# Kernel tuning notes

Measured on AMD Instinct MI355X. Metric: run time of the kernel, lower is better.

The kernel has to match this reference:

```python
import jax, jax.numpy as jnp
import numpy as np

EMBED_DIM = 1024
LN_EPS = 1e-5


def _layernorm(x, w, b):
    m = jnp.mean(x, axis=-1, keepdims=True)
    v = jnp.mean(jnp.square(x - m), axis=-1, keepdims=True)
    return (x - m) * jax.lax.rsqrt(v + LN_EPS) * w + b


def _attention(q, k, v, scale):
    # q: [b, sq, d], k/v: [b, sk, d]
    scores = jnp.einsum('bqd,bkd->bqk', q, k) * scale
    probs = jax.nn.softmax(scores, axis=-1)
    return jnp.einsum('bqk,bkd->bqd', probs, v)


def setup_inputs() -> dict:
    key = jax.random.key(0)
    ks = jax.random.split(key, 16)
    B, SQ, SK, D, H = 8, 577, 13271, EMBED_DIM, 4  # H=int(4.0) per source
    return {
        'input_features': jax.random.normal(ks[0], (B, SK, D), jnp.float32),
        'query_feature': jax.random.normal(ks[1], (B, SQ, D), jnp.float32),
        'norm1_w': jax.random.uniform(ks[2], (D,), jnp.float32, 0.5, 1.5),
        'norm1_b': jax.random.normal(ks[3], (D,), jnp.float32) * 0.1,
        'norm2_w': jax.random.uniform(ks[4], (D,), jnp.float32, 0.5, 1.5),
        'norm2_b': jax.random.normal(ks[5], (D,), jnp.float32) * 0.1,
        'norm3_w': jax.random.uniform(ks[6], (D,), jnp.float32, 0.5, 1.5),
        'norm3_b': jax.random.normal(ks[7], (D,), jnp.float32) * 0.1,
        'gamma1': jax.random.uniform(ks[8], (D,), jnp.float32, 0.5, 1.5),
        'gamma2': jax.random.uniform(ks[9], (D,), jnp.float32, 0.5, 1.5),
        'fc1_w': jax.random.normal(ks[10], (H, D), jnp.float32) * (1.0 / np.sqrt(D)),
        'fc1_b': jax.random.normal(ks[11], (H,), jnp.float32) * 0.01,
        'fc2_w': jax.random.normal(ks[12], (D, H), jnp.float32) * (1.0 / np.sqrt(H)),
        'fc2_b': jax.random.normal(ks[13], (D,), jnp.float32) * 0.01,
    }


def reference(input_features, query_feature, norm1_w, norm1_b, norm2_w, norm2_b,
              norm3_w, norm3_b, gamma1, gamma2, fc1_w, fc1_b, fc2_w, fc2_b):
    scale = EMBED_DIM ** (-0.5)
    norm_X = _layernorm(input_features, norm1_w, norm1_b)
    norm_F_L = _layernorm(query_feature, norm2_w, norm2_b)
    # cross attention: query = last-layer feats, key/value = concat of earlier layers
    attended = _attention(norm_F_L, norm_X, norm_X, scale)
    # MLP with exact-erf GELU (torch nn.GELU default), dropout=0 -> identity
    h = jax.nn.gelu(attended @ fc1_w.T + fc1_b, approximate=False)
    cross_attended = h @ fc2_w.T + fc2_b
    norm_cross = _layernorm(cross_attended, norm3_w, norm3_b)
    self_attended = _attention(norm_cross, norm_cross, norm_cross, scale)
    skip_connect = cross_attended + gamma1 * self_attended
    return norm_F_L + gamma2 * skip_connect
```

## Files before the change

### kernel.cpp

```cpp
#include <hip/hip_runtime.h>
#include <hip/hip_bf16.h>
#include <math.h>

typedef unsigned short u16;
typedef __attribute__((ext_vector_type(4))) unsigned short u16x4;
typedef __attribute__((ext_vector_type(8))) __bf16 bf16x8;
typedef __attribute__((ext_vector_type(4))) float fx4;

#define DEV __device__ __forceinline__

DEV u16 f2bf(float f) {
    unsigned u = __float_as_uint(f);
    u += 0x7fffu + ((u >> 16) & 1u);
    return (u16)(u >> 16);
}

DEV void async_load16(const void* g, void* l) {
    __builtin_amdgcn_global_load_lds(
        (const __attribute__((address_space(1))) void*)g,
        (__attribute__((address_space(3))) void*)l, 16, 0, 0);
}

DEV void block_reduce2(float& a, float& b) {
    #pragma unroll
    for (int o = 32; o; o >>= 1) { a += __shfl_xor(a, o); b += __shfl_xor(b, o); }
    __shared__ float sa[4], sb[4];
    const int lane = threadIdx.x & 63, wv = threadIdx.x >> 6;
    if (lane == 0) { sa[wv] = a; sb[wv] = b; }
    __syncthreads();
    a = sa[0] + sa[1] + sa[2] + sa[3];
    b = sb[0] + sb[1] + sb[2] + sb[3];
    __syncthreads();
}

DEV void xcd_swizzle3(int& bx, int& by, int& bz) {
    const int nx = gridDim.x, ny = gridDim.y;
    const int total = nx * ny * gridDim.z;
    const int lin = blockIdx.x + nx * (blockIdx.y + ny * blockIdx.z);
    if (total & 7) { bx = blockIdx.x; by = blockIdx.y; bz = blockIdx.z; return; }
    const int cpx = total >> 3;
    const int swz = (lin & 7) * cpx + (lin >> 3);
    bx = swz % nx;
    const int r = swz / nx;
    by = r % ny;
    bz = r / ny;
}

__global__ __launch_bounds__(256) void ln_wave_k(
    const float* __restrict__ in, int rows_real, int rows_pad,
    const float* __restrict__ w, const float* __restrict__ bias,
    u16* __restrict__ out_bf, float* __restrict__ out_f32, float out_scale)
{
    const int wv = threadIdx.x >> 6, lane = threadIdx.x & 63;
    const int r = blockIdx.x * 4 + wv, b = blockIdx.y;
    const size_t orow = ((size_t)b * rows_pad + r) * 1024 + lane * 4;
    if (r >= rows_real) {
        u16x4 z = {0, 0, 0, 0};
        fx4 zf = {0.f, 0.f, 0.f, 0.f};
        #pragma unroll
        for (int c = 0; c < 4; ++c) {
            *(u16x4*)&out_bf[orow + c * 256] = z;
            if (out_f32) *(fx4*)&out_f32[orow + c * 256] = zf;
        }
        return;
    }
    const size_t irow = ((size_t)b * rows_real + r) * 1024 + lane * 4;
    fx4 x[4];
    float s1 = 0.f, s2 = 0.f;
    #pragma unroll
    for (int c = 0; c < 4; ++c) {
        x[c] = *(const fx4*)&in[irow + c * 256];
        s1 += x[c].x + x[c].y + x[c].z + x[c].w;
        s2 += x[c].x * x[c].x + x[c].y * x[c].y + x[c].z * x[c].z + x[c].w * x[c].w;
    }
    #pragma unroll
    for (int o = 32; o; o >>= 1) { s1 += __shfl_xor(s1, o); s2 += __shfl_xor(s2, o); }
    const float m = s1 * (1.0f / 1024.0f);
    const float var = s2 * (1.0f / 1024.0f) - m * m;
    const float rs = rsqrtf(var + 1e-5f);
    #pragma unroll
    for (int c = 0; c < 4; ++c) {
        fx4 wv4 = *(const fx4*)&w[c * 256 + lane * 4];
        fx4 bv4 = *(const fx4*)&bias[c * 256 + lane * 4];
        fx4 y;
        y.x = (x[c].x - m) * rs * wv4.x + bv4.x;
        y.y = (x[c].y - m) * rs * wv4.y + bv4.y;
        y.z = (x[c].z - m) * rs * wv4.z + bv4.z;
        y.w = (x[c].w - m) * rs * wv4.w + bv4.w;
        u16x4 o = { f2bf(y.x * out_scale), f2bf(y.y * out_scale),
                    f2bf(y.z * out_scale), f2bf(y.w * out_scale) };
        *(u16x4*)&out_bf[orow + c * 256] = o;
        if (out_f32) *(fx4*)&out_f32[orow + c * 256] = y;
    }
}

template<bool ATOMIC>
DEV void gemm_body(
    const u16* __restrict__ Ab, const u16* __restrict__ Bb, float* __restrict__ Cb,
    int k_begin, int iters, int lda, int ldb, int ldc)
{
    __shared__ u16 lA[2][128 * 32];
    __shared__ u16 lB[2][128 * 32];
    const int lane = threadIdx.x & 63, wv = threadIdx.x >> 6;
    const int wm = (wv >> 1) * 64, wn = (wv & 1) * 64;
    const int frow = lane & 15, quad = lane >> 4;

    fx4 acc[4][4];
    #pragma unroll
    for (int i = 0; i < 4; ++i)
        #pragma unroll
        for (int j = 0; j < 4; ++j) { acc[i][j].x = 0; acc[i][j].y = 0; acc[i][j].z = 0; acc[i][j].w = 0; }

    const int c0 = wv * 64 + lane;
    const int r0a = c0 >> 2, s0 = (c0 & 3) * 8;
    const int c1 = 256 + c0;
    const int r1a = c1 >> 2, s1 = (c1 & 3) * 8;

    auto stage = [&](int buf, int it) {
        const int k0 = k_begin + it * 32;
        async_load16(Ab + (size_t)r0a * lda + k0 + s0, &lA[buf][(wv * 64) * 8]);
        async_load16(Ab + (size_t)r1a * lda + k0 + s1, &lA[buf][(256 + wv * 64) * 8]);
        async_load16(Bb + (size_t)r0a * ldb + k0 + s0, &lB[buf][(wv * 64) * 8]);
        async_load16(Bb + (size_t)r1a * ldb + k0 + s1, &lB[buf][(256 + wv * 64) * 8]);
    };

    stage(0, 0);
    __syncthreads();
    int cur = 0;
    for (int it = 0; it < iters; ++it) {
        if (it + 1 < iters) stage(cur ^ 1, it + 1);
        bf16x8 af[4], bfr[4];
        #pragma unroll
        for (int i = 0; i < 4; ++i) {
            af[i]  = *(const bf16x8*)&lA[cur][(wm + i * 16 + frow) * 32 + quad * 8];
            bfr[i] = *(const bf16x8*)&lB[cur][(wn + i * 16 + frow) * 32 + quad * 8];
        }
        #pragma unroll
        for (int mi = 0; mi < 4; ++mi)
            #pragma unroll
            for (int ni = 0; ni < 4; ++ni)
                acc[mi][ni] = __builtin_amdgcn_mfma_f32_16x16x32_bf16(af[mi], bfr[ni], acc[mi][ni], 0, 0, 0);
        __syncthreads();
        cur ^= 1;
    }

    #pragma unroll
    for (int mi = 0; mi < 4; ++mi) {
        #pragma unroll
        for (int r = 0; r < 4; ++r) {
            const int row = wm + mi * 16 + quad * 4 + r;
            #pragma unroll
            for (int ni = 0; ni < 4; ++ni) {
                const int col = wn + ni * 16 + frow;
                if (ATOMIC) atomicAdd(&Cb[(size_t)row * ldc + col], acc[mi][ni][r]);
                else        Cb[(size_t)row * ldc + col] = acc[mi][ni][r];
            }
        }
    }
}

template<int NS>
__global__ __launch_bounds__(256) void gemm_bt_sk(
    const u16* __restrict__ A, const u16* __restrict__ B, float* __restrict__ C,
    int iters_per, int lda, int ldb, int ldc, long As, long Bs, long Cs)
{
    int bx, by, bzz;
    xcd_swizzle3(bx, by, bzz);
    const int bz = bzz / NS, sp = bzz % NS;
    const u16* Ab = A + (size_t)bz * As + (size_t)by * 128 * lda;
    const u16* Bb = B + (size_t)bz * Bs + (size_t)bx * 128 * ldb;
    float* Cb = C + (size_t)bz * Cs + (size_t)by * 128 * ldc + (size_t)bx * 128;
    gemm_body<true>(Ab, Bb, Cb, sp * iters_per * 32, iters_per, lda, ldb, ldc);
}

template<bool ATOMIC>
DEV void gemm256_body(
    const u16* __restrict__ A, const u16* __restrict__ B, float* __restrict__ C,
    int k_begin, int NT, int lda, int ldb, int ldc, int bx, int by, int Mreal)
{
    __shared__ u16 lds[2][4][8192];
    const int tid = threadIdx.x;
    const int lane = tid & 63, wid = tid >> 6;
    const int wr = wid >> 2, wc = wid & 3;
    const int frow = lane & 15, quad = lane >> 4;
    const int sw = (frow & 7) << 4;
    const int csrc = ((lane & 7) ^ ((lane >> 3) & 7)) * 8;
    const int by256 = by * 256, bx256 = bx * 256;
    const int mclamp = Mreal - 1;

    fx4 acc[8][4];
    #pragma unroll
    for (int i = 0; i < 8; ++i)
        #pragma unroll
        for (int j = 0; j < 4; ++j) { acc[i][j].x = 0; acc[i][j].y = 0; acc[i][j].z = 0; acc[i][j].w = 0; }

    auto stageA = [&](int buf, int half, int ktile) {
        const int kcol = k_begin + ktile * 64;
        #pragma unroll
        for (int j = 0; j < 2; ++j) {
            int grow = by256 + half * 128 + (wid * 2 + j) * 8 + (lane >> 3);
            if (grow > mclamp) grow = mclamp;
            async_load16(A + (size_t)grow * lda + kcol + csrc,
                         &lds[buf][half][(wid * 2 + j) * 512]);
        }
    };
    auto stageB = [&](int buf, int half, int ktile) {
        const int kcol = k_begin + ktile * 64;
        #pragma unroll
        for (int j = 0; j < 2; ++j) {
            const int grow = bx256 + half * 128 + (wid * 2 + j) * 8 + (lane >> 3);
            async_load16(B + (size_t)grow * ldb + kcol + csrc,
                         &lds[buf][2 + half][(wid * 2 + j) * 512]);
        }
    };

#define DO_PHASE(MQ, NQ, STAGE_STMT, WAITN)                                              \
    {                                                                                    \
        STAGE_STMT;                                                                      \
        __builtin_amdgcn_sched_barrier(0);                                               \
        asm volatile("s_waitcnt vmcnt(" #WAITN ")" ::: "memory");                        \
        __builtin_amdgcn_s_barrier();                                                    \
        __builtin_amdgcn_sched_barrier(0);                                               \
        const char* pa = (const char*)&lds[cur][MQ][0];                                  \
        const char* pb = (const char*)&lds[cur][2 + NQ][0];                              \
        bf16x8 av[4][2], bv[2][2];                                                       \
        _Pragma("unroll")                                                                \
        for (int f = 0; f < 4; ++f) {                                                    \
            const int row = wr * 64 + f * 16 + frow;                                     \
            _Pragma("unroll")                                                            \
            for (int ks = 0; ks < 2; ++ks)                                               \
                av[f][ks] = *(const bf16x8*)(pa + row * 128 + ((((ks * 4 + quad) << 4)) ^ sw)); \
        }                                                                                \
        _Pragma("unroll")                                                                \
        for (int gg = 0; gg < 2; ++gg) {                                                 \
            const int col = wc * 32 + gg * 16 + frow;                                    \
            _Pragma("unroll")                                                            \
            for (int ks = 0; ks < 2; ++ks)                                               \
                bv[gg][ks] = *(const bf16x8*)(pb + col * 128 + ((((ks * 4 + quad) << 4)) ^ sw)); \
        }                                                                                \
        __builtin_amdgcn_s_setprio(1);                                                   \
        _Pragma("unroll")                                                                \
        for (int f = 0; f < 4; ++f)                                                      \
            _Pragma("unroll")                                                            \
            for (int gg = 0; gg < 2; ++gg)                                               \
                _Pragma("unroll")                                                        \
                for (int ks = 0; ks < 2; ++ks)                                           \
                    acc[MQ * 4 + f][NQ * 2 + gg] = __builtin_amdgcn_mfma_f32_16x16x32_bf16( \
                        av[f][ks], bv[gg][ks], acc[MQ * 4 + f][NQ * 2 + gg], 0, 0, 0);   \
        __builtin_amdgcn_s_setprio(0);                                                   \
    }

    stageA(0, 0, 0);
    stageB(0, 0, 0);
    stageB(0, 1, 0);
    stageA(0, 1, 0);
    stageA(1, 0, 1);

    int cur = 0;
    for (int t = 0; t <= NT - 2; ++t) {
        const int nxt = cur ^ 1;
        DO_PHASE(0, 0, stageB(nxt, 0, t + 1), 8)
        DO_PHASE(0, 1, stageB(nxt, 1, t + 1), 8)
        DO_PHASE(1, 0, stageA(nxt, 1, t + 1), 8)
        DO_PHASE(1, 1, if (t + 2 < NT) stageA(cur, 0, t + 2), 8)
        cur = nxt;
    }
    DO_PHASE(0, 0, (void)0, 4)
    DO_PHASE(0, 1, (void)0, 2)
    DO_PHASE(1, 0, (void)0, 0)
    DO_PHASE(1, 1, (void)0, 0)
#undef DO_PHASE

    #pragma unroll
    for (int mf = 0; mf < 8; ++mf) {
        const int rowb = (mf >> 2) * 128 + wr * 64 + (mf & 3) * 16 + quad * 4;
        #pragma unroll
        for (int r = 0; r < 4; ++r) {
            const int grow = by256 + rowb + r;
            if (grow < Mreal) {
                #pragma unroll
                for (int nf = 0; nf < 4; ++nf) {
                    const int gcol = bx256 + (nf >> 1) * 128 + wc * 32 + (nf & 1) * 16 + frow;
                    if (ATOMIC) atomicAdd(&C[(size_t)grow * ldc + gcol], acc[mf][nf][r]);
                    else C[(size_t)grow * ldc + gcol] = acc[mf][nf][r];
                }
            }
        }
    }
}

__global__ __launch_bounds__(512, 2) void gemm256_qk(
    const u16* __restrict__ A, const u16* __restrict__ B, float* __restrict__ C,
    int NT, int lda, int ldb, int ldc, long As, long Bs, long Cs, int Mreal)
{
    const int lin = blockIdx.x + gridDim.x * (blockIdx.y + gridDim.y * blockIdx.z);
    const int per_bx = gridDim.y * gridDim.z;
    const int bx = lin / per_bx, rem = lin % per_bx;
    const int by = rem % gridDim.y, bz = rem / gridDim.y;
    gemm256_body<false>(A + (size_t)bz * As, B + (size_t)bz * Bs, C + (size_t)bz * Cs,
                        0, NT, lda, ldb, ldc, bx, by, Mreal);
}

template<int NS>
__global__ __launch_bounds__(512, 2) void gemm256_sk(
    const u16* __restrict__ A, const u16* __restrict__ B, float* __restrict__ C,
    int NT_per, int lda, int ldb, int ldc, long As, long Bs, long Cs, int Mreal)
{
    int bx, by, bzz;
    xcd_swizzle3(bx, by, bzz);
    const int bz = bzz / NS, sp = bzz % NS;
    gemm256_body<true>(A + (size_t)bz * As, B + (size_t)bz * Bs, C + (size_t)bz * Cs,
                       sp * NT_per * 64, NT_per, lda, ldb, ldc, bx, by, Mreal);
}

template<int EPT4>
__global__ __launch_bounds__(256) void softmax_k(
    const float* __restrict__ S, u16* __restrict__ P,
    int n_real, int n_pad, float scale, long Ss, long Ps)
{
    const int tid = threadIdx.x;
    const float* Sr = S + (size_t)blockIdx.y * Ss + (size_t)blockIdx.x * n_pad;
    u16* Pr = P + (size_t)blockIdx.y * Ps + (size_t)blockIdx.x * n_pad;
    fx4 v[EPT4];
    float mx = -INFINITY;
    #pragma unroll
    for (int i = 0; i < EPT4; ++i) {
        const int base = (i * 256 + tid) * 4;
        fx4 s;
        if (base < n_pad) s = *(const fx4*)&Sr[base];
        else { s.x = -INFINITY; s.y = -INFINITY; s.z = -INFINITY; s.w = -INFINITY; }
        s.x = (base + 0 < n_real) ? s.x * scale : -INFINITY;
        s.y = (base + 1 < n_real) ? s.y * scale : -INFINITY;
        s.z = (base + 2 < n_real) ? s.z * scale : -INFINITY;
        s.w = (base + 3 < n_real) ? s.w * scale : -INFINITY;
        v[i] = s;
        mx = fmaxf(mx, fmaxf(fmaxf(s.x, s.y), fmaxf(s.z, s.w)));
    }
    #pragma unroll
    for (int o = 32; o; o >>= 1) mx = fmaxf(mx, __shfl_xor(mx, o));
    __shared__ float sm[4];
    const int lane = tid & 63, wvi = tid >> 6;
    if (lane == 0) sm[wvi] = mx;
    __syncthreads();
    mx = fmaxf(fmaxf(sm[0], sm[1]), fmaxf(sm[2], sm[3]));
    __syncthreads();
    float sum = 0.f;
    #pragma unroll
    for (int i = 0; i < EPT4; ++i) {
        fx4 e;
        e.x = __expf(v[i].x - mx); e.y = __expf(v[i].y - mx);
        e.z = __expf(v[i].z - mx); e.w = __expf(v[i].w - mx);
        v[i] = e;
        sum += e.x + e.y + e.z + e.w;
    }
    #pragma unroll
    for (int o = 32; o; o >>= 1) sum += __shfl_xor(sum, o);
    if (lane == 0) sm[wvi] = sum;
    __syncthreads();
    sum = sm[0] + sm[1] + sm[2] + sm[3];
    const float inv = 1.0f / sum;
    #pragma unroll
    for (int i = 0; i < EPT4; ++i) {
        const int base = (i * 256 + tid) * 4;
        if (base < n_pad) {
            u16x4 o = { f2bf(v[i].x * inv), f2bf(v[i].y * inv),
                        f2bf(v[i].z * inv), f2bf(v[i].w * inv) };
            *(u16x4*)&Pr[base] = o;
        }
    }
}

__global__ __launch_bounds__(256) void transpose_k(
    const u16* __restrict__ in, u16* __restrict__ out,
    int in_rows, int in_cols, long is, long os)
{
    __shared__ u16 t[64][68];
    const int b = blockIdx.z;
    const u16* I = in + (size_t)b * is;
    u16* O = out + (size_t)b * os;
    const int c0 = blockIdx.x * 64, r0 = blockIdx.y * 64;
    const int cx = threadIdx.x & 15, ry = threadIdx.x >> 4;
    u16x4 a[4];
    #pragma unroll
    for (int k = 0; k < 4; ++k)
        a[k] = *(const u16x4*)&I[(size_t)(r0 + 4 * ry + k) * in_cols + c0 + 4 * cx];
    #pragma unroll
    for (int e = 0; e < 4; ++e) {
        u16x4 o = { a[0][e], a[1][e], a[2][e], a[3][e] };
        *(u16x4*)&t[4 * cx + e][4 * ry] = o;
    }
    __syncthreads();
    #pragma unroll
    for (int k = 0; k < 4; ++k) {
        const int oc = 4 * ry + k;
        *(u16x4*)&O[(size_t)(c0 + oc) * in_rows + r0 + 4 * cx] =
            *(const u16x4*)&t[oc][4 * cx];
    }
}

__global__ __launch_bounds__(256) void mlp_ln_k(
    const float* __restrict__ att, const float* __restrict__ w1, const float* __restrict__ b1,
    const float* __restrict__ w2, const float* __restrict__ b2,
    const float* __restrict__ w3, const float* __restrict__ b3,
    float* __restrict__ ca, u16* __restrict__ nc, int rows_real)
{
    const int q = blockIdx.x, b = blockIdx.y, tid = threadIdx.x;
    const size_t row = ((size_t)b * gridDim.x + q) * 1024 + tid * 4;
    if (q >= rows_real) {
        fx4 zf = {0.f, 0.f, 0.f, 0.f}; u16x4 z = {0, 0, 0, 0};
        *(fx4*)&ca[row] = zf;
        *(u16x4*)&nc[row] = z;
        return;
    }
    fx4 x = *(const fx4*)&att[row];
    float p[4];
    #pragma unroll
    for (int j = 0; j < 4; ++j) {
        fx4 wj = *(const fx4*)&w1[j * 1024 + tid * 4];
        p[j] = x.x * wj.x + x.y * wj.y + x.z * wj.z + x.w * wj.w;
        #pragma unroll
        for (int o = 32; o; o >>= 1) p[j] += __shfl_xor(p[j], o);
    }
    __shared__ float sh[4][4];
    const int lane = tid & 63, wvi = tid >> 6;
    if (lane == 0) { sh[wvi][0] = p[0]; sh[wvi][1] = p[1]; sh[wvi][2] = p[2]; sh[wvi][3] = p[3]; }
    __syncthreads();
    float h[4];
    #pragma unroll
    for (int j = 0; j < 4; ++j) {
        float s = sh[0][j] + sh[1][j] + sh[2][j] + sh[3][j] + b1[j];
        h[j] = 0.5f * s * (1.0f + erff(s * 0.70710678118f));
    }
    float v[4]; float s1 = 0.f, s2 = 0.f;
    #pragma unroll
    for (int e = 0; e < 4; ++e) {
        const int d = tid * 4 + e;
        fx4 wd = *(const fx4*)&w2[d * 4];
        float t = h[0] * wd.x + h[1] * wd.y + h[2] * wd.z + h[3] * wd.w + b2[d];
        v[e] = t; s1 += t; s2 += t * t;
    }
    block_reduce2(s1, s2);
    const float m = s1 * (1.0f / 1024.0f);
    const float var = s2 * (1.0f / 1024.0f) - m * m;
    const float rs = rsqrtf(var + 1e-5f);
    fx4 cav = {v[0], v[1], v[2], v[3]};
    *(fx4*)&ca[row] = cav;
    fx4 w3v = *(const fx4*)&w3[tid * 4], b3v = *(const fx4*)&b3[tid * 4];
    u16x4 o = { f2bf((v[0] - m) * rs * w3v.x + b3v.x), f2bf((v[1] - m) * rs * w3v.y + b3v.y),
                f2bf((v[2] - m) * rs * w3v.z + b3v.z), f2bf((v[3] - m) * rs * w3v.w + b3v.w) };
    *(u16x4*)&nc[row] = o;
}

__global__ __launch_bounds__(256) void final_k(
    const float* __restrict__ nF, const float* __restrict__ ca,
    const float* __restrict__ att2, const float* __restrict__ g1,
    const float* __restrict__ g2, float* __restrict__ out, int sq, int sqp)
{
    const int q = blockIdx.x, b = blockIdx.y, tid = threadIdx.x;
    const size_t wrow = ((size_t)b * sqp + q) * 1024 + tid * 4;
    const size_t orow = ((size_t)b * sq + q) * 1024 + tid * 4;
    fx4 nf = *(const fx4*)&nF[wrow];
    fx4 c  = *(const fx4*)&ca[wrow];
    fx4 a2 = *(const fx4*)&att2[wrow];
    fx4 G1 = *(const fx4*)&g1[tid * 4];
    fx4 G2 = *(const fx4*)&g2[tid * 4];
    fx4 r;
    r.x = nf.x + G2.x * (c.x + G1.x * a2.x);
    r.y = nf.y + G2.y * (c.y + G1.y * a2.y);
    r.z = nf.z + G2.z * (c.z + G1.z * a2.z);
    r.w = nf.w + G2.w * (c.w + G1.w * a2.w);
    *(fx4*)&out[orow] = r;
}

extern "C" void kernel_launch(void* const* d_in, const int* in_sizes, int n_in,
                              void* d_out, int out_size, void* d_ws, size_t ws_size,
                              hipStream_t stream) {
    const float* x_in = (const float*)d_in[0];
    const float* q_in = (const float*)d_in[1];
    const float* n1w = (const float*)d_in[2];
    const float* n1b = (const float*)d_in[3];
    const float* n2w = (const float*)d_in[4];
    const float* n2b = (const float*)d_in[5];
    const float* n3w = (const float*)d_in[6];
    const float* n3b = (const float*)d_in[7];
    const float* g1  = (const float*)d_in[8];
    const float* g2  = (const float*)d_in[9];
    const float* w1  = (const float*)d_in[10];
    const float* b1  = (const float*)d_in[11];
    const float* w2  = (const float*)d_in[12];
    const float* b2  = (const float*)d_in[13];
    float* out = (float*)d_out;

    const int B = 8, SQ = 577, SK = 13271, D = 1024;
    const int SQP = 640, SKP = 13312;
    const float scale = 0.03125f;

    char* ws = (char*)d_ws;
    size_t off = 0;
    auto alloc = [&](size_t n) { size_t o = off; off = (off + n + 255) & ~(size_t)255; return o; };
    u16*   Xn   = (u16*)  (ws + alloc((size_t)B * SKP * D * 2));
    u16*   Xt   = (u16*)  (ws + alloc((size_t)B * D * SKP * 2));
    u16*   Qb   = (u16*)  (ws + alloc((size_t)B * SQP * D * 2));
    float* nF   = (float*)(ws + alloc((size_t)B * SQP * D * 4));
    u16*   P    = (u16*)  (ws + alloc((size_t)B * SQP * SKP * 2));
    float* att  = (float*)(ws + alloc((size_t)B * SQP * D * 4));
    float* CA   = (float*)(ws + alloc((size_t)B * SQP * D * 4));
    u16*   NC   = (u16*)  (ws + alloc((size_t)B * SQP * D * 2));
    u16*   NCt  = (u16*)  (ws + alloc((size_t)B * D * SQP * 2));
    float* S2   = (float*)(ws + alloc((size_t)B * SQP * SQP * 4));
    u16*   P2   = (u16*)  (ws + alloc((size_t)B * SQP * SQP * 2));
    float* att2 = (float*)(ws + alloc((size_t)B * SQP * D * 4));
    const size_t perS1 = (size_t)SQP * SKP * 4;
    size_t room = (ws_size > off) ? (ws_size - off) / perS1 : 1;
    int g = (int)(room < 1 ? 1 : (room > 4 ? 4 : room));
    float* S1 = (float*)(ws + off);
    (void)in_sizes; (void)n_in; (void)out_size;

    ln_wave_k<<<dim3(SKP / 4, B), 256, 0, stream>>>(x_in, SK, SKP, n1w, n1b, Xn, nullptr, 1.0f);
    ln_wave_k<<<dim3(SQP / 4, B), 256, 0, stream>>>(q_in, SQ, SQP, n2w, n2b, Qb, nF, scale);

    transpose_k<<<dim3(D / 64, SKP / 64, B), 256, 0, stream>>>(
        Xn, Xt, SKP, D, (long)SKP * D, (long)SKP * D);

    for (int b = 0; b < B; b += g) {
        const int nb = (B - b) < g ? (B - b) : g;
        gemm256_qk<<<dim3(SKP / 256, 3, nb), 512, 0, stream>>>(
            Qb + (size_t)b * SQP * D, Xn + (size_t)b * SKP * D, S1,
            D / 64, D, D, SKP, (long)SQP * D, (long)SKP * D, (long)SQP * SKP, SQP);
        softmax_k<13><<<dim3(SQP, nb), 256, 0, stream>>>(
            S1, P + (size_t)b * SQP * SKP, SK, SKP, 1.0f,
            (long)SQP * SKP, (long)SQP * SKP);
    }

    hipMemsetAsync(att, 0, (size_t)B * SQP * D * 4, stream);
    gemm256_sk<8><<<dim3(D / 256, 3, B * 8), 512, 0, stream>>>(
        P, Xt, att, (SKP / 64) / 8, SKP, SKP, D,
        (long)SQP * SKP, (long)D * SKP, (long)SQP * D, SQP);

    mlp_ln_k<<<dim3(SQP, B), 256, 0, stream>>>(att, w1, b1, w2, b2, n3w, n3b, CA, NC, SQ);

    transpose_k<<<dim3(D / 64, SQP / 64, B), 256, 0, stream>>>(
        NC, NCt, SQP, D, (long)SQP * D, (long)SQP * D);
    hipMemsetAsync(S2, 0, (size_t)B * SQP * SQP * 4, stream);
    gemm_bt_sk<2><<<dim3(SQP / 128, SQP / 128, B * 2), 256, 0, stream>>>(
        NC, NC, S2, 16, D, D, SQP,
        (long)SQP * D, (long)SQP * D, (long)SQP * SQP);
    softmax_k<1><<<dim3(SQP, B), 256, 0, stream>>>(
        S2, P2, SQ, SQP, scale, (long)SQP * SQP, (long)SQP * SQP);
    hipMemsetAsync(att2, 0, (size_t)B * SQP * D * 4, stream);
    gemm_bt_sk<4><<<dim3(D / 128, SQP / 128, B * 4), 256, 0, stream>>>(
        P2, NCt, att2, 5, SQP, SQP, D,
        (long)SQP * SQP, (long)D * SQP, (long)SQP * D);

    final_k<<<dim3(SQ, B), 256, 0, stream>>>(nF, CA, att2, g1, g2, out, SQ, SQP);
}
```

Measured before the change: 1.344 ms.

## Read untransposed Xn in PV GEMM via LDS transpose loads; drop transpose kernel

Removes the transpose of the normalized keys/values (Xn to Xt) and has the split-K P·V GEMM stage B tiles straight from the row-major Xn. Fragments are then read with ds_read_b64_tr_b16 transpose reads from a swizzled LDS layout. This cuts a full read and write pass over a roughly 200 MB bf16 tensor and frees its workspace. It also raises the QK batch-group cap from 4 to 8, so that freed space can hold more S1 buffers. The cost is an explicit lgkmcnt wait and inline asm in the inner phase, plus adjusted vmcnt counts that must match the new load pattern.

New measurement: 1.275 ms. 5.2% less time.

```diff
diff --git a/kernel.cpp b/kernel.cpp
--- a/kernel.cpp
+++ b/kernel.cpp
@@ -5,6 +5,7 @@
 typedef unsigned short u16;
 typedef __attribute__((ext_vector_type(4))) unsigned short u16x4;
 typedef __attribute__((ext_vector_type(8))) __bf16 bf16x8;
+typedef __attribute__((ext_vector_type(4))) __bf16 bf16x4;
 typedef __attribute__((ext_vector_type(4))) float fx4;
 
 #define DEV __device__ __forceinline__
@@ -173,7 +174,7 @@
     gemm_body<true>(Ab, Bb, Cb, sp * iters_per * 32, iters_per, lda, ldb, ldc);
 }
 
-template<bool ATOMIC>
+template<bool ATOMIC, bool BTRANS>
 DEV void gemm256_body(
     const u16* __restrict__ A, const u16* __restrict__ B, float* __restrict__ C,
     int k_begin, int NT, int lda, int ldb, int ldc, int bx, int by, int Mreal)
@@ -187,6 +188,8 @@
     const int csrc = ((lane & 7) ^ ((lane >> 3) & 7)) * 8;
     const int by256 = by * 256, bx256 = bx * 256;
     const int mclamp = Mreal - 1;
+    const unsigned ldsb0 = (unsigned)(size_t)(__attribute__((address_space(3))) void*)&lds[0][2][0];
+    const unsigned ldsb1 = (unsigned)(size_t)(__attribute__((address_space(3))) void*)&lds[1][2][0];
 
     fx4 acc[8][4];
     #pragma unroll
@@ -194,7 +197,7 @@
         #pragma unroll
         for (int j = 0; j < 4; ++j) { acc[i][j].x = 0; acc[i][j].y = 0; acc[i][j].z = 0; acc[i][j].w = 0; }
 
-    auto stageA = [&](int buf, int half, int ktile) {
+    auto stA = [&](int buf, int half, int ktile) {
         const int kcol = k_begin + ktile * 64;
         #pragma unroll
         for (int j = 0; j < 2; ++j) {
@@ -204,13 +207,24 @@
                          &lds[buf][half][(wid * 2 + j) * 512]);
         }
     };
-    auto stageB = [&](int buf, int half, int ktile) {
-        const int kcol = k_begin + ktile * 64;
-        #pragma unroll
-        for (int j = 0; j < 2; ++j) {
-            const int grow = bx256 + half * 128 + (wid * 2 + j) * 8 + (lane >> 3);
-            async_load16(B + (size_t)grow * ldb + kcol + csrc,
-                         &lds[buf][2 + half][(wid * 2 + j) * 512]);
+    auto stB = [&](int buf, int half, int ktile) {
+        if constexpr (BTRANS) {
+            const int kb = k_begin + ktile * 64 + half * 32;
+            #pragma unroll
+            for (int j = 0; j < 2; ++j) {
+                const int rl = (wid * 2 + j) * 2 + (lane >> 5);
+                const int cc = (lane & 31) ^ (rl & 7);
+                async_load16(B + (size_t)(kb + rl) * ldb + bx256 + cc * 8,
+                             &lds[buf][2 + half][(wid * 2 + j) * 512]);
+            }
+        } else {
+            const int kcol = k_begin + ktile * 64;
+            #pragma unroll
+            for (int j = 0; j < 2; ++j) {
+                const int grow = bx256 + half * 128 + (wid * 2 + j) * 8 + (lane >> 3);
+                async_load16(B + (size_t)grow * ldb + kcol + csrc,
+                             &lds[buf][2 + half][(wid * 2 + j) * 512]);
+            }
         }
     };
 
@@ -218,11 +232,10 @@
     {                                                                                    \
         STAGE_STMT;                                                                      \
         __builtin_amdgcn_sched_barrier(0);                                               \
-        asm volatile("s_waitcnt vmcnt(" #WAITN ")" ::: "memory");                        \
+        asm volatile("s_waitcnt vmcnt(%0)" :: "i"(WAITN) : "memory");                    \
         __builtin_amdgcn_s_barrier();                                                    \
         __builtin_amdgcn_sched_barrier(0);                                               \
         const char* pa = (const char*)&lds[cur][MQ][0];                                  \
-        const char* pb = (const char*)&lds[cur][2 + NQ][0];                              \
         bf16x8 av[4][2], bv[2][2];                                                       \
         _Pragma("unroll")                                                                \
         for (int f = 0; f < 4; ++f) {                                                    \
@@ -231,12 +244,33 @@
             for (int ks = 0; ks < 2; ++ks)                                               \
                 av[f][ks] = *(const bf16x8*)(pa + row * 128 + ((((ks * 4 + quad) << 4)) ^ sw)); \
         }                                                                                \
-        _Pragma("unroll")                                                                \
-        for (int gg = 0; gg < 2; ++gg) {                                                 \
-            const int col = wc * 32 + gg * 16 + frow;                                    \
+        if constexpr (BTRANS) {                                                          \
+            const unsigned bB = cur ? ldsb1 : ldsb0;                                     \
             _Pragma("unroll")                                                            \
-            for (int ks = 0; ks < 2; ++ks)                                               \
-                bv[gg][ks] = *(const bf16x8*)(pb + col * 128 + ((((ks * 4 + quad) << 4)) ^ sw)); \
+            for (int gg = 0; gg < 2; ++gg)                                               \
+                _Pragma("unroll")                                                        \
+                for (int ks = 0; ks < 2; ++ks) {                                         \
+                    const int rlo = ks * 32 + quad * 8 + ((lane & 15) >> 2);             \
+                    const int ob = ((NQ) * 128 + wc * 32 + gg * 16 + 4 * (lane & 3)) * 2;\
+                    const unsigned alo = bB + rlo * 512 + (ob ^ ((rlo & 7) << 4));       \
+                    const unsigned ahi = bB + (rlo + 4) * 512 + (ob ^ (((rlo + 4) & 7) << 4)); \
+                    bf16x4 plo, phi;                                                     \
+                    asm volatile("ds_read_b64_tr_b16 %0, %2\n\t"                        \
+                                 "ds_read_b64_tr_b16 %1, %3"                            \
+                                 : "=v"(plo), "=v"(phi) : "v"(alo), "v"(ahi));           \
+                    bv[gg][ks] = __builtin_shufflevector(plo, phi, 0, 1, 2, 3, 4, 5, 6, 7); \
+                }                                                                        \
+            asm volatile("s_waitcnt lgkmcnt(0)" ::: "memory");                           \
+            __builtin_amdgcn_sched_barrier(0);                                           \
+        } else {                                                                         \
+            const char* pb = (const char*)&lds[cur][2 + NQ][0];                          \
+            _Pragma("unroll")                                                            \
+            for (int gg = 0; gg < 2; ++gg) {                                             \
+                const int col = wc * 32 + gg * 16 + frow;                                \
+                _Pragma("unroll")                                                        \
+                for (int ks = 0; ks < 2; ++ks)                                           \
+                    bv[gg][ks] = *(const bf16x8*)(pb + col * 128 + ((((ks * 4 + quad) << 4)) ^ sw)); \
+            }                                                                            \
         }                                                                                \
         __builtin_amdgcn_s_setprio(1);                                                   \
         _Pragma("unroll")                                                                \
@@ -250,22 +284,22 @@
         __builtin_amdgcn_s_setprio(0);                                                   \
     }
 
-    stageA(0, 0, 0);
-    stageB(0, 0, 0);
-    stageB(0, 1, 0);
-    stageA(0, 1, 0);
-    stageA(1, 0, 1);
+    stA(0, 0, 0);
+    stB(0, 0, 0);
+    stB(0, 1, 0);
+    stA(0, 1, 0);
+    stA(1, 0, 1);
 
     int cur = 0;
     for (int t = 0; t <= NT - 2; ++t) {
         const int nxt = cur ^ 1;
-        DO_PHASE(0, 0, stageB(nxt, 0, t + 1), 8)
-        DO_PHASE(0, 1, stageB(nxt, 1, t + 1), 8)
-        DO_PHASE(1, 0, stageA(nxt, 1, t + 1), 8)
-        DO_PHASE(1, 1, if (t + 2 < NT) stageA(cur, 0, t + 2), 8)
+        DO_PHASE(0, 0, stB(nxt, 0, t + 1), (BTRANS ? 6 : 8))
+        DO_PHASE(0, 1, stB(nxt, 1, t + 1), 8)
+        DO_PHASE(1, 0, stA(nxt, 1, t + 1), 8)
+        DO_PHASE(1, 1, if (t + 2 < NT) stA(cur, 0, t + 2), 8)
         cur = nxt;
     }
-    DO_PHASE(0, 0, (void)0, 4)
+    DO_PHASE(0, 0, (void)0, (BTRANS ? 2 : 4))
     DO_PHASE(0, 1, (void)0, 2)
     DO_PHASE(1, 0, (void)0, 0)
     DO_PHASE(1, 1, (void)0, 0)
@@ -297,8 +331,8 @@
     const int per_bx = gridDim.y * gridDim.z;
     const int bx = lin / per_bx, rem = lin % per_bx;
     const int by = rem % gridDim.y, bz = rem / gridDim.y;
-    gemm256_body<false>(A + (size_t)bz * As, B + (size_t)bz * Bs, C + (size_t)bz * Cs,
-                        0, NT, lda, ldb, ldc, bx, by, Mreal);
+    gemm256_body<false, false>(A + (size_t)bz * As, B + (size_t)bz * Bs, C + (size_t)bz * Cs,
+                               0, NT, lda, ldb, ldc, bx, by, Mreal);
 }
 
 template<int NS>
@@ -309,8 +343,8 @@
     int bx, by, bzz;
     xcd_swizzle3(bx, by, bzz);
     const int bz = bzz / NS, sp = bzz % NS;
-    gemm256_body<true>(A + (size_t)bz * As, B + (size_t)bz * Bs, C + (size_t)bz * Cs,
-                       sp * NT_per * 64, NT_per, lda, ldb, ldc, bx, by, Mreal);
+    gemm256_body<true, true>(A + (size_t)bz * As, B + (size_t)bz * Bs, C + (size_t)bz * Cs,
+                             sp * NT_per * 64, NT_per, lda, ldb, ldc, bx, by, Mreal);
 }
 
 template<int EPT4>
@@ -499,7 +533,6 @@
     size_t off = 0;
     auto alloc = [&](size_t n) { size_t o = off; off = (off + n + 255) & ~(size_t)255; return o; };
     u16*   Xn   = (u16*)  (ws + alloc((size_t)B * SKP * D * 2));
-    u16*   Xt   = (u16*)  (ws + alloc((size_t)B * D * SKP * 2));
     u16*   Qb   = (u16*)  (ws + alloc((size_t)B * SQP * D * 2));
     float* nF   = (float*)(ws + alloc((size_t)B * SQP * D * 4));
     u16*   P    = (u16*)  (ws + alloc((size_t)B * SQP * SKP * 2));
@@ -512,15 +545,12 @@
     float* att2 = (float*)(ws + alloc((size_t)B * SQP * D * 4));
     const size_t perS1 = (size_t)SQP * SKP * 4;
     size_t room = (ws_size > off) ? (ws_size - off) / perS1 : 1;
-    int g = (int)(room < 1 ? 1 : (room > 4 ? 4 : room));
+    int g = (int)(room < 1 ? 1 : (room > 8 ? 8 : room));
     float* S1 = (float*)(ws + off);
     (void)in_sizes; (void)n_in; (void)out_size;
 
     ln_wave_k<<<dim3(SKP / 4, B), 256, 0, stream>>>(x_in, SK, SKP, n1w, n1b, Xn, nullptr, 1.0f);
     ln_wave_k<<<dim3(SQP / 4, B), 256, 0, stream>>>(q_in, SQ, SQP, n2w, n2b, Qb, nF, scale);
-
-    transpose_k<<<dim3(D / 64, SKP / 64, B), 256, 0, stream>>>(
-        Xn, Xt, SKP, D, (long)SKP * D, (long)SKP * D);
 
     for (int b = 0; b < B; b += g) {
         const int nb = (B - b) < g ? (B - b) : g;
@@ -534,8 +564,8 @@
 
     hipMemsetAsync(att, 0, (size_t)B * SQP * D * 4, stream);
     gemm256_sk<8><<<dim3(D / 256, 3, B * 8), 512, 0, stream>>>(
-        P, Xt, att, (SKP / 64) / 8, SKP, SKP, D,
-        (long)SQP * SKP, (long)D * SKP, (long)SQP * D, SQP);
+        P, Xn, att, (SKP / 64) / 8, SKP, D, D,
+        (long)SQP * SKP, (long)SKP * D, (long)SQP * D, SQP);
 
     mlp_ln_k<<<dim3(SQP, B), 256, 0, stream>>>(att, w1, b1, w2, b2, n3w, n3b, CA, NC, SQ);
 
```
